# Kernel tuning notes

Hardware: AMD Instinct MI355X
Metric: run time of the kernel (lower is better)

Reference implementation:

```python
import jax, jax.numpy as jnp
import numpy as np
from itertools import permutations

B, Nm, S, K, H, OUT = 32, 128, 16, 4, 128, 1
LG, LI, LGL = 3, 2, 2  # num_layer, num_layer_id, num_layer_global
EPS = 1e-5


def _ln(x, g, b):
    m = jnp.mean(x, -1, keepdims=True)
    v = jnp.mean(jnp.square(x - m), -1, keepdims=True)
    return (x - m) * jax.lax.rsqrt(v + EPS) * g + b


def _block(x, W1, b1, W2, b2, g, bn):
    # Linear -> ReLU -> Linear -> LayerNorm -> ReLU
    h = jax.nn.relu(x @ W1 + b1)
    return jax.nn.relu(_ln(h @ W2 + b2, g, bn))


def setup_inputs() -> dict:
    key = jax.random.key(0)
    ks = iter(jax.random.split(key, 64))
    nrm = lambda shape, s=0.05: jax.random.normal(next(ks), shape, jnp.float32) * s
    x = nrm((B, Nm, 1), 1.0)
    adj = (jax.random.uniform(next(ks), (B, Nm, Nm)) < 0.05).astype(jnp.float32)
    # allperm: all permutations of [1..K-1] with 0 prepended, transposed -> (K, permdim)
    ap = np.array(list(permutations(range(1, K))), dtype=np.int32)
    ap = np.concatenate([np.zeros((ap.shape[0], 1), np.int32), ap], axis=1).T
    allperm = jnp.asarray(ap)
    Ssub = B * S
    base = jax.random.randint(next(ks), (Ssub,), 0, Nm - K)
    subgs = base[:, None] + jnp.arange(K, dtype=jnp.int32)[None, :]  # distinct nodes per subgraph
    num_subg = jnp.full((B,), S, jnp.int32)
    num_node = jnp.full((B,), Nm, jnp.int32)
    d = dict(x=x, adj=adj,
             idemb=nrm((K + 2, H)),
             in_W1=nrm((1, H)), in_b1=jnp.zeros((H,)), in_W2=nrm((H, H)), in_b2=jnp.zeros((H,)),
             in_g=jnp.ones((H,)), in_bn=jnp.zeros((H,)),
             gW1=nrm((LG, H, H)), gb1=jnp.zeros((LG, H)), gW2=nrm((LG, H, H)), gb2=jnp.zeros((LG, H)),
             gg=jnp.ones((LG, H)), gbn=jnp.zeros((LG, H)),
             iW1=nrm((LI, H, H)), ib1=jnp.zeros((LI, H)), iW2=nrm((LI, H, H)), ib2=jnp.zeros((LI, H)),
             ig=jnp.ones((LI, H)), ibn=jnp.zeros((LI, H)),
             glW1=nrm((LGL, H, H)), glb1=jnp.zeros((LGL, H)), glW2=nrm((LGL, H, H)), glb2=jnp.zeros((LGL, H)),
             glg=jnp.ones((LGL, H)), glbn=jnp.zeros((LGL, H)),
             s1_W=nrm((H, H)), s1_b=jnp.zeros((H,)), s2_W=nrm((H, H)), s2_b=jnp.zeros((H,)),
             rW1=nrm((H, H)), rb1=jnp.zeros((H,)), rW2=nrm((H, H)), rb2=jnp.zeros((H,)),
             rg=jnp.ones((H,)), rbn=jnp.zeros((H,)),
             out_W=nrm((H, OUT)), out_b=jnp.zeros((OUT,)),
             subgs=subgs, num_subg=num_subg, num_node=num_node, allperm=allperm)
    return d


def reference(x, adj, idemb, in_W1, in_b1, in_W2, in_b2, in_g, in_bn,
              gW1, gb1, gW2, gb2, gg, gbn,
              iW1, ib1, iW2, ib2, ig, ibn,
              glW1, glb1, glW2, glb2, glg, glbn,
              s1_W, s1_b, s2_W, s2_b,
              rW1, rb1, rW2, rb2, rg, rbn,
              out_W, out_b, subgs, num_subg, num_node, allperm):
    Bsz, N = x.shape[0], x.shape[1]
    Ssub, k = subgs.shape
    permdim = allperm.shape[1]
    # input embedding MLP
    h = _block(x, in_W1, in_b1, in_W2, in_b2, in_g, in_bn)  # (B, Nm, H)
    Hd = h.shape[-1]
    # subgraph -> graph batch map (ns_b = S per graph; Ssub static)
    subgbatch = jnp.repeat(jnp.arange(Bsz), num_subg, total_repeat_length=Ssub)
    # identity labeling: z starts as ones, labeled nodes get idemb(allperm[pos])
    lb = jnp.repeat(jnp.arange(Ssub), k)          # label batch (subgraph idx)
    lnodes = subgs.reshape(-1)                    # node ids within graph
    ni = jnp.tile(jnp.arange(k), Ssub)            # position within subgraph
    vals = idemb[allperm[ni]]                     # (Ssub*k, permdim, H)
    z = jnp.ones((Ssub, N, permdim, Hd), x.dtype)
    z = z.at[lb, lnodes].multiply(vals)
    # graph message passing on full graphs
    for l in range(gW1.shape[0]):
        m = jnp.einsum('bij,bjd->bid', adj, h)
        h = h + _block(m, gW1[l], gb1[l], gW2[l], gb2[l], gg[l], gbn[l])
    hs = h[subgbatch]        # (Ssub, Nm, H)
    sadj = adj[subgbatch]    # (Ssub, Nm, Nm)
    # id message passing over permutation channels
    for l in range(iW1.shape[0]):
        m = jnp.einsum('bij,bjpd->bipd', sadj, z)
        z = z + _block(m, iW1[l], ib1[l], iW2[l], ib2[l], ig[l], ibn[l])
    # zero out padded (null) nodes
    null_mask = jnp.arange(N)[None, :] >= num_node[:, None]  # (B, Nm)
    z = jnp.where(null_mask[subgbatch][:, :, None, None], 0.0, z)
    z = jax.nn.relu(z.mean(axis=2) @ s1_W + s1_b)  # setmlp1, (Ssub, Nm, H)
    hs = hs + z
    for l in range(glW1.shape[0]):
        m = jnp.einsum('bij,bjd->bid', sadj, hs)
        hs = hs + _block(m, glW1[l], glb1[l], glW2[l], glb2[l], glg[l], glbn[l])
    hs = jax.nn.relu(hs.sum(axis=1) @ s2_W + s2_b)  # setmlp2, (Ssub, H)
    pooled = jax.ops.segment_max(hs, subgbatch, num_segments=Bsz)  # global max pool
    pooled = pooled + _block(pooled, rW1, rb1, rW2, rb2, rg, rbn)  # setmlp3 (1 layer)
    return pooled @ out_W + out_b  # (B, OUT)
```

## Files before the change

### kernel.cpp

```cpp
#include <hip/hip_runtime.h>
#include <hip/hip_bf16.h>
#include <string.h>

typedef __hip_bfloat16 bf16;
typedef short v8s __attribute__((ext_vector_type(8)));
typedef float v4f __attribute__((ext_vector_type(4)));

#define H_ 128
#define P_ 6
#define K_ 4

__device__ __forceinline__ float s2f(short s) {
    unsigned int u = ((unsigned int)(unsigned short)s) << 16;
    float f; __builtin_memcpy(&f, &u, 4); return f;
}
__device__ __forceinline__ short f2s(float v) {
    bf16 h = __float2bfloat16(v);
    short s; __builtin_memcpy(&s, &h, 2); return s;
}
__device__ __forceinline__ v4f MFMA(v8s a, v8s b, v4f c) {
    return __builtin_amdgcn_mfma_f32_16x16x32_bf16(a, b, c, 0, 0, 0);
}

__global__ __launch_bounds__(128) void k_prep(const float* __restrict__ adj,
    float* __restrict__ degf, bf16* __restrict__ adjb,
    const float* __restrict__ iW1, const float* __restrict__ iW2,
    const float* __restrict__ glW1, const float* __restrict__ glW2,
    const float* __restrict__ in_W2, const float* __restrict__ gW1,
    const float* __restrict__ gW2, const float* __restrict__ s1_W,
    bf16* __restrict__ WT, bf16* __restrict__ WT2, bf16* __restrict__ s1Wt)
{
    __shared__ float red[128];
    const int b = blockIdx.x, t = threadIdx.x;
    if (b < 4096) {
        float a = adj[(size_t)b * 128 + t];
        adjb[(size_t)b * 128 + t] = __float2bfloat16(a);
        red[t] = a;
        __syncthreads();
        for (int s = 64; s > 0; s >>= 1) {
            if (t < s) red[t] += red[t + s];
            __syncthreads();
        }
        if (t == 0) degf[b] = red[0];
    } else if (b < 5120) {
        const int bb = b - 4096, w = bb >> 7, n = bb & 127;
        const float* arr[8] = {iW1, iW2, iW1 + 16384, iW2 + 16384,
                               glW1, glW2, glW1 + 16384, glW2 + 16384};
        WT[(size_t)w * 16384 + n * 128 + t] = __float2bfloat16(arr[w][t * 128 + n]);
    } else if (b < 6144) {
        const int bb = b - 5120, w = bb >> 7, n = bb & 127;
        const float* arr[8] = {in_W2, gW1, gW2, gW1 + 16384,
                               gW2 + 16384, gW1 + 32768, gW2 + 32768, in_W2};
        WT2[(size_t)w * 16384 + n * 128 + t] = __float2bfloat16(arr[w][t * 128 + n]);
    } else {
        const int n = b - 6144;
        s1Wt[n * 128 + t] = __float2bfloat16(s1_W[t * 128 + n]);
    }
}

__global__ __launch_bounds__(256) void k_id1h(
    const float* __restrict__ adj, const float* __restrict__ degf,
    const int* __restrict__ subgs, const int* __restrict__ allperm,
    const float* __restrict__ idemb, bf16* __restrict__ outb,
    const bf16* __restrict__ W1t, const float* __restrict__ b1,
    const bf16* __restrict__ W2t, const float* __restrict__ b2,
    const float* __restrict__ gam, const float* __restrict__ bet,
    const float* __restrict__ x, const bf16* __restrict__ adjb,
    const float* __restrict__ inW1, const float* __restrict__ inb1,
    const bf16* __restrict__ inW2t, const float* __restrict__ inb2,
    const float* __restrict__ ing, const float* __restrict__ inbn,
    const bf16* __restrict__ WTg,
    const float* __restrict__ gb1, const float* __restrict__ gb2,
    const float* __restrict__ gg, const float* __restrict__ gbn,
    float* __restrict__ hb)
{
    __shared__ __align__(16) short sB[128][136];
    __shared__ float sP[15][128];
    const int t = threadIdx.x;
    const int wave = t >> 6, lane = t & 63, quad = lane >> 4, l16 = lane & 15;
    const int wrow = wave << 5;

    if (blockIdx.x < 3072) {
        const int bi = blockIdx.x;
        const int b_s = bi / 6, p = bi - b_s * 6;
        const int g = b_s >> 4;
        float (*sE)[128] = sP;

        int nodeq[K_];
        #pragma unroll
        for (int q = 0; q < K_; ++q) nodeq[q] = subgs[b_s * K_ + q];

        for (int u = t; u < K_ * 128; u += 256) {
            const int q = u >> 7, f = u & 127;
            sE[q][f] = idemb[(size_t)allperm[q * P_ + p] * H_ + f] - 1.f;
        }
        __syncthreads();

        {
            const int i = t >> 1, half = (t & 1) * 64;
            const int gi = g * 128 + i;
            const float dg = degf[gi];
            float aq[K_];
            #pragma unroll
            for (int q = 0; q < K_; ++q) aq[q] = adj[(size_t)gi * 128 + nodeq[q]];
            #pragma unroll
            for (int f = 0; f < 64; ++f) {
                float v = dg;
                #pragma unroll
                for (int q = 0; q < K_; ++q) v = fmaf(aq[q], sE[q][half + f], v);
                sB[i][half + f] = f2s(v);
            }
        }
        __syncthreads();

        v4f acc[2][8];
        #pragma unroll
        for (int mt = 0; mt < 2; ++mt)
            #pragma unroll
            for (int nt = 0; nt < 8; ++nt) acc[mt][nt] = (v4f){0.f, 0.f, 0.f, 0.f};
        #pragma unroll
        for (int kk = 0; kk < 4; ++kk) {
            v8s a0 = *(const v8s*)&sB[wrow + l16][kk * 32 + quad * 8];
            v8s a1 = *(const v8s*)&sB[wrow + 16 + l16][kk * 32 + quad * 8];
            #pragma unroll
            for (int nt = 0; nt < 8; ++nt) {
                v8s b = *(const v8s*)(W1t + (nt * 16 + l16) * 128 + kk * 32 + quad * 8);
                acc[0][nt] = MFMA(a0, b, acc[0][nt]);
                acc[1][nt] = MFMA(a1, b, acc[1][nt]);
            }
        }
        #pragma unroll
        for (int nt = 0; nt < 8; ++nt) {
            float bb = b1[nt * 16 + l16];
            #pragma unroll
            for (int mt = 0; mt < 2; ++mt)
                #pragma unroll
                for (int r = 0; r < 4; ++r)
                    sB[wrow + mt * 16 + quad * 4 + r][nt * 16 + l16] = f2s(fmaxf(acc[mt][nt][r] + bb, 0.f));
        }
        #pragma unroll
        for (int mt = 0; mt < 2; ++mt)
            #pragma unroll
            for (int nt = 0; nt < 8; ++nt) acc[mt][nt] = (v4f){0.f, 0.f, 0.f, 0.f};
        #pragma unroll
        for (int kk = 0; kk < 4; ++kk) {
            v8s a0 = *(const v8s*)&sB[wrow + l16][kk * 32 + quad * 8];
            v8s a1 = *(const v8s*)&sB[wrow + 16 + l16][kk * 32 + quad * 8];
            #pragma unroll
            for (int nt = 0; nt < 8; ++nt) {
                v8s b = *(const v8s*)(W2t + (nt * 16 + l16) * 128 + kk * 32 + quad * 8);
                acc[0][nt] = MFMA(a0, b, acc[0][nt]);
                acc[1][nt] = MFMA(a1, b, acc[1][nt]);
            }
        }
        float bb2[8], gv[8], bv[8];
        #pragma unroll
        for (int nt = 0; nt < 8; ++nt) {
            int n = nt * 16 + l16;
            bb2[nt] = b2[n]; gv[nt] = gam[n]; bv[nt] = bet[n];
        }
        #pragma unroll
        for (int mt = 0; mt < 2; ++mt)
            #pragma unroll
            for (int r = 0; r < 4; ++r) {
                float s = 0.f, q = 0.f;
                #pragma unroll
                for (int nt = 0; nt < 8; ++nt) {
                    float u = acc[mt][nt][r] + bb2[nt];
                    acc[mt][nt][r] = u;
                    s += u; q += u * u;
                }
                #pragma unroll
                for (int d = 1; d < 16; d <<= 1) {
                    s += __shfl_xor(s, d);
                    q += __shfl_xor(q, d);
                }
                float mn = s * (1.f / 128.f);
                float rs = rsqrtf(q * (1.f / 128.f) - mn * mn + 1e-5f);
                #pragma unroll
                for (int nt = 0; nt < 8; ++nt) {
                    float v = fmaxf((acc[mt][nt][r] - mn) * rs * gv[nt] + bv[nt], 0.f);
                    sB[wrow + mt * 16 + quad * 4 + r][nt * 16 + l16] = f2s(v + 1.0f);
                }
            }
        __syncthreads();
        {
            const int f = t >> 1, nh = (t & 1) * 64;
            const short* flat = &sB[0][0];
            bf16* dst = outb + (size_t)bi * 16384 + (size_t)f * 128 + nh;
            #pragma unroll
            for (int u = 0; u < 8; ++u) {
                v8s pk;
                #pragma unroll
                for (int e = 0; e < 8; ++e) pk[e] = flat[(nh + u * 8 + e) * 136 + f];
                *(v8s*)(dst + u * 8) = pk;
            }
        }
        return;
    }

    const int g = blockIdx.x - 3072;

    for (int u = t; u < 15 * 128; u += 256) {
        const int a = u >> 7, n = u & 127;
        const float* src;
        if (a == 0) src = inb2;
        else if (a == 1) src = ing;
        else if (a == 2) src = inbn;
        else {
            const int l = (a - 3) >> 2, pp = (a - 3) & 3;
            src = (pp == 0) ? gb1 + l * 128 : (pp == 1) ? gb2 + l * 128
                : (pp == 2) ? gg + l * 128 : gbn + l * 128;
        }
        sP[a][n] = src[n];
    }

    v8s aA[2][4];
    {
        const bf16* ar = adjb + (size_t)g * 16384;
        #pragma unroll
        for (int mt = 0; mt < 2; ++mt)
            #pragma unroll
            for (int kk = 0; kk < 4; ++kk)
                aA[mt][kk] = *(const v8s*)(ar + (size_t)(wrow + mt * 16 + l16) * 128 + kk * 32 + quad * 8);
    }

    {
        const int i = t >> 1, half = (t & 1) * 64;
        const float xv = x[(size_t)g * 128 + i];
        #pragma unroll
        for (int fb = 0; fb < 64; fb += 8) {
            v8s pk;
            #pragma unroll
            for (int e = 0; e < 8; ++e)
                pk[e] = f2s(fmaxf(fmaf(xv, inW1[half + fb + e], inb1[half + fb + e]), 0.f));
            *(v8s*)&sB[i][half + fb] = pk;
        }
    }
    v4f acc[2][8];
    #pragma unroll
    for (int mt = 0; mt < 2; ++mt)
        #pragma unroll
        for (int nt = 0; nt < 8; ++nt) acc[mt][nt] = (v4f){0.f, 0.f, 0.f, 0.f};
    #pragma unroll
    for (int kk = 0; kk < 4; ++kk) {
        v8s a0 = *(const v8s*)&sB[wrow + l16][kk * 32 + quad * 8];
        v8s a1 = *(const v8s*)&sB[wrow + 16 + l16][kk * 32 + quad * 8];
        #pragma unroll
        for (int nt = 0; nt < 8; ++nt) {
            v8s b = *(const v8s*)(inW2t + (nt * 16 + l16) * 128 + kk * 32 + quad * 8);
            acc[0][nt] = MFMA(a0, b, acc[0][nt]);
            acc[1][nt] = MFMA(a1, b, acc[1][nt]);
        }
    }
    __syncthreads();
    float hs_reg[2][8][4];
    #pragma unroll
    for (int mt = 0; mt < 2; ++mt)
        #pragma unroll
        for (int r = 0; r < 4; ++r) {
            float s = 0.f, qq = 0.f;
            #pragma unroll
            for (int nt = 0; nt < 8; ++nt) {
                float u = acc[mt][nt][r] + sP[0][nt * 16 + l16];
                acc[mt][nt][r] = u;
                s += u; qq += u * u;
            }
            #pragma unroll
            for (int d = 1; d < 16; d <<= 1) {
                s += __shfl_xor(s, d);
                qq += __shfl_xor(qq, d);
            }
            float mn = s * (1.f / 128.f);
            float rs = rsqrtf(qq * (1.f / 128.f) - mn * mn + 1e-5f);
            const int i = wrow + mt * 16 + quad * 4 + r;
            #pragma unroll
            for (int nt = 0; nt < 8; ++nt) {
                const int n = nt * 16 + l16;
                float v = fmaxf((acc[mt][nt][r] - mn) * rs * sP[1][n] + sP[2][n], 0.f);
                hs_reg[mt][nt][r] = v;
                sB[n][i] = f2s(v);
            }
        }
    __syncthreads();

    for (int l = 0; l < 3; ++l) {
        const bf16* W1t_ = WTg + (size_t)(2 * l) * 16384;
        const bf16* W2t_ = WTg + (size_t)(2 * l + 1) * 16384;
        #pragma unroll
        for (int mt = 0; mt < 2; ++mt)
            #pragma unroll
            for (int nt = 0; nt < 8; ++nt) acc[mt][nt] = (v4f){0.f, 0.f, 0.f, 0.f};
        #pragma unroll
        for (int kk = 0; kk < 4; ++kk)
            #pragma unroll
            for (int nt = 0; nt < 8; ++nt) {
                v8s b = *(const v8s*)&sB[nt * 16 + l16][kk * 32 + quad * 8];
                acc[0][nt] = MFMA(aA[0][kk], b, acc[0][nt]);
                acc[1][nt] = MFMA(aA[1][kk], b, acc[1][nt]);
            }
        __syncthreads();
        #pragma unroll
        for (int nt = 0; nt < 8; ++nt)
            #pragma unroll
            for (int mt = 0; mt < 2; ++mt)
                #pragma unroll
                for (int r = 0; r < 4; ++r)
                    sB[wrow + mt * 16 + quad * 4 + r][nt * 16 + l16] = f2s(acc[mt][nt][r]);
        #pragma unroll
        for (int mt = 0; mt < 2; ++mt)
            #pragma unroll
            for (int nt = 0; nt < 8; ++nt) acc[mt][nt] = (v4f){0.f, 0.f, 0.f, 0.f};
        #pragma unroll
        for (int kk = 0; kk < 4; ++kk) {
            v8s a0 = *(const v8s*)&sB[wrow + l16][kk * 32 + quad * 8];
            v8s a1 = *(const v8s*)&sB[wrow + 16 + l16][kk * 32 + quad * 8];
            #pragma unroll
            for (int nt = 0; nt < 8; ++nt) {
                v8s b = *(const v8s*)(W1t_ + (nt * 16 + l16) * 128 + kk * 32 + quad * 8);
                acc[0][nt] = MFMA(a0, b, acc[0][nt]);
                acc[1][nt] = MFMA(a1, b, acc[1][nt]);
            }
        }
        #pragma unroll
        for (int nt = 0; nt < 8; ++nt) {
            float bb = sP[3 + 4 * l + 0][nt * 16 + l16];
            #pragma unroll
            for (int mt = 0; mt < 2; ++mt)
                #pragma unroll
                for (int r = 0; r < 4; ++r)
                    sB[wrow + mt * 16 + quad * 4 + r][nt * 16 + l16] = f2s(fmaxf(acc[mt][nt][r] + bb, 0.f));
        }
        #pragma unroll
        for (int mt = 0; mt < 2; ++mt)
            #pragma unroll
            for (int nt = 0; nt < 8; ++nt) acc[mt][nt] = (v4f){0.f, 0.f, 0.f, 0.f};
        #pragma unroll
        for (int kk = 0; kk < 4; ++kk) {
            v8s a0 = *(const v8s*)&sB[wrow + l16][kk * 32 + quad * 8];
            v8s a1 = *(const v8s*)&sB[wrow + 16 + l16][kk * 32 + quad * 8];
            #pragma unroll
            for (int nt = 0; nt < 8; ++nt) {
                v8s b = *(const v8s*)(W2t_ + (nt * 16 + l16) * 128 + kk * 32 + quad * 8);
                acc[0][nt] = MFMA(a0, b, acc[0][nt]);
                acc[1][nt] = MFMA(a1, b, acc[1][nt]);
            }
        }
        __syncthreads();
        #pragma unroll
        for (int mt = 0; mt < 2; ++mt)
            #pragma unroll
            for (int r = 0; r < 4; ++r) {
                float s = 0.f, qq = 0.f;
                #pragma unroll
                for (int nt = 0; nt < 8; ++nt) {
                    float u = acc[mt][nt][r] + sP[3 + 4 * l + 1][nt * 16 + l16];
                    acc[mt][nt][r] = u;
                    s += u; qq += u * u;
                }
                #pragma unroll
                for (int d = 1; d < 16; d <<= 1) {
                    s += __shfl_xor(s, d);
                    qq += __shfl_xor(qq, d);
                }
                float mn = s * (1.f / 128.f);
                float rs = rsqrtf(qq * (1.f / 128.f) - mn * mn + 1e-5f);
                const int i = wrow + mt * 16 + quad * 4 + r;
                #pragma unroll
                for (int nt = 0; nt < 8; ++nt) {
                    const int n = nt * 16 + l16;
                    float v = fmaxf((acc[mt][nt][r] - mn) * rs * sP[3 + 4 * l + 2][n] + sP[3 + 4 * l + 3][n], 0.f);
                    float h2 = hs_reg[mt][nt][r] + v;
                    hs_reg[mt][nt][r] = h2;
                    sB[n][i] = f2s(h2);
                }
            }
        __syncthreads();
    }

    #pragma unroll
    for (int mt = 0; mt < 2; ++mt)
        #pragma unroll
        for (int nt = 0; nt < 8; ++nt)
            #pragma unroll
            for (int r = 0; r < 4; ++r) {
                const int i = wrow + mt * 16 + quad * 4 + r;
                const int n = nt * 16 + l16;
                hb[((size_t)(g * 128 + i)) * 128 + n] = hs_reg[mt][nt][r];
            }
}

__global__ __launch_bounds__(256) void k_id2_v9(
    const bf16* __restrict__ z2t, bf16* __restrict__ zm,
    const bf16* __restrict__ adjb, const int* __restrict__ num_node,
    const int* __restrict__ subgs, const int* __restrict__ allperm,
    const float* __restrict__ idemb,
    const bf16* __restrict__ W1t, const float* __restrict__ b1,
    const bf16* __restrict__ W2t, const float* __restrict__ b2,
    const float* __restrict__ gam, const float* __restrict__ bet)
{
    __shared__ __align__(16) short sB[128][136];
    __shared__ float sP[4][128];
    const int t = threadIdx.x;
    const int b_s = blockIdx.x;
    const int g = b_s >> 4;
    const int wave = t >> 6, lane = t & 63, quad = lane >> 4, l16 = lane & 15;
    const int wrow = wave << 5;

    #pragma unroll
    for (int u = 0; u < 2; ++u) {
        const int v = t + u * 256;
        const int a = v >> 7, n = v & 127;
        const float* src = (a == 0) ? b1 : (a == 1) ? b2 : (a == 2) ? gam : bet;
        sP[a][n] = src[n];
    }

    v8s aA[2][4];
    {
        const bf16* ar = adjb + (size_t)g * 16384;
        #pragma unroll
        for (int mt = 0; mt < 2; ++mt)
            #pragma unroll
            for (int kk = 0; kk < 4; ++kk)
                aA[mt][kk] = *(const v8s*)(ar + (size_t)(wrow + mt * 16 + l16) * 128 + kk * 32 + quad * 8);
    }
    int nodeq[K_];
    #pragma unroll
    for (int q = 0; q < K_; ++q) nodeq[q] = subgs[b_s * K_ + q];

    float macc[2][8][4];
    #pragma unroll
    for (int mt = 0; mt < 2; ++mt)
        #pragma unroll
        for (int nt = 0; nt < 8; ++nt)
            #pragma unroll
            for (int r = 0; r < 4; ++r) macc[mt][nt][r] = 0.f;

    const int sf = t >> 1, shalf = (t & 1) * 64;

    for (int p = 0; p < P_; ++p) {
        {
            const bf16* src = z2t + ((size_t)(b_s * P_ + p)) * 16384 + (size_t)sf * 128 + shalf;
            #pragma unroll
            for (int u = 0; u < 8; ++u)
                *(v8s*)&sB[sf][shalf + u * 8] = *(const v8s*)(src + u * 8);
        }
        __syncthreads();
        if (t < 128) {
            #pragma unroll
            for (int q = 0; q < K_; ++q) {
                float e = idemb[(size_t)allperm[q * P_ + p] * H_ + t] - 1.f;
                short* cell = &sB[t][nodeq[q]];
                *cell = f2s(s2f(*cell) + e);
            }
        }
        __syncthreads();
        #pragma unroll
        for (int mt = 0; mt < 2; ++mt)
            #pragma unroll
            for (int nt = 0; nt < 8; ++nt) {
                const int n = nt * 16 + l16;
                #pragma unroll
                for (int r = 0; r < 4; ++r)
                    macc[mt][nt][r] += s2f(sB[n][wrow + mt * 16 + quad * 4 + r]);
            }
        v4f acc[2][8];
        #pragma unroll
        for (int mt = 0; mt < 2; ++mt)
            #pragma unroll
            for (int nt = 0; nt < 8; ++nt) acc[mt][nt] = (v4f){0.f, 0.f, 0.f, 0.f};
        #pragma unroll
        for (int kk = 0; kk < 4; ++kk)
            #pragma unroll
            for (int nt = 0; nt < 8; ++nt) {
                v8s b = *(const v8s*)&sB[nt * 16 + l16][kk * 32 + quad * 8];
                acc[0][nt] = MFMA(aA[0][kk], b, acc[0][nt]);
                acc[1][nt] = MFMA(aA[1][kk], b, acc[1][nt]);
            }
        __syncthreads();
        #pragma unroll
        for (int nt = 0; nt < 8; ++nt)
            #pragma unroll
            for (int mt = 0; mt < 2; ++mt)
                #pragma unroll
                for (int r = 0; r < 4; ++r)
                    sB[wrow + mt * 16 + quad * 4 + r][nt * 16 + l16] = f2s(acc[mt][nt][r]);
        #pragma unroll
        for (int mt = 0; mt < 2; ++mt)
            #pragma unroll
            for (int nt = 0; nt < 8; ++nt) acc[mt][nt] = (v4f){0.f, 0.f, 0.f, 0.f};
        #pragma unroll
        for (int kk = 0; kk < 4; ++kk) {
            v8s a0 = *(const v8s*)&sB[wrow + l16][kk * 32 + quad * 8];
            v8s a1 = *(const v8s*)&sB[wrow + 16 + l16][kk * 32 + quad * 8];
            #pragma unroll
            for (int nt = 0; nt < 8; ++nt) {
                v8s b = *(const v8s*)(W1t + (nt * 16 + l16) * 128 + kk * 32 + quad * 8);
                acc[0][nt] = MFMA(a0, b, acc[0][nt]);
                acc[1][nt] = MFMA(a1, b, acc[1][nt]);
            }
        }
        #pragma unroll
        for (int nt = 0; nt < 8; ++nt) {
            float bb = sP[0][nt * 16 + l16];
            #pragma unroll
            for (int mt = 0; mt < 2; ++mt)
                #pragma unroll
                for (int r = 0; r < 4; ++r)
                    sB[wrow + mt * 16 + quad * 4 + r][nt * 16 + l16] = f2s(fmaxf(acc[mt][nt][r] + bb, 0.f));
        }
        #pragma unroll
        for (int mt = 0; mt < 2; ++mt)
            #pragma unroll
            for (int nt = 0; nt < 8; ++nt) acc[mt][nt] = (v4f){0.f, 0.f, 0.f, 0.f};
        #pragma unroll
        for (int kk = 0; kk < 4; ++kk) {
            v8s a0 = *(const v8s*)&sB[wrow + l16][kk * 32 + quad * 8];
            v8s a1 = *(const v8s*)&sB[wrow + 16 + l16][kk * 32 + quad * 8];
            #pragma unroll
            for (int nt = 0; nt < 8; ++nt) {
                v8s b = *(const v8s*)(W2t + (nt * 16 + l16) * 128 + kk * 32 + quad * 8);
                acc[0][nt] = MFMA(a0, b, acc[0][nt]);
                acc[1][nt] = MFMA(a1, b, acc[1][nt]);
            }
        }
        #pragma unroll
        for (int mt = 0; mt < 2; ++mt)
            #pragma unroll
            for (int r = 0; r < 4; ++r) {
                float s = 0.f, qq = 0.f;
                #pragma unroll
                for (int nt = 0; nt < 8; ++nt) {
                    float u = acc[mt][nt][r] + sP[1][nt * 16 + l16];
                    acc[mt][nt][r] = u;
                    s += u; qq += u * u;
                }
                #pragma unroll
                for (int d = 1; d < 16; d <<= 1) {
                    s += __shfl_xor(s, d);
                    qq += __shfl_xor(qq, d);
                }
                float mn = s * (1.f / 128.f);
                float rs = rsqrtf(qq * (1.f / 128.f) - mn * mn + 1e-5f);
                #pragma unroll
                for (int nt = 0; nt < 8; ++nt) {
                    const int n = nt * 16 + l16;
                    macc[mt][nt][r] += fmaxf((acc[mt][nt][r] - mn) * rs * sP[2][n] + sP[3][n], 0.f);
                }
            }
        __syncthreads();
    }
    const int nn = num_node[g];
    #pragma unroll
    for (int mt = 0; mt < 2; ++mt)
        #pragma unroll
        for (int nt = 0; nt < 8; ++nt)
            #pragma unroll
            for (int r = 0; r < 4; ++r) {
                const int i = wrow + mt * 16 + quad * 4 + r;
                const int n = nt * 16 + l16;
                float v = (i >= nn) ? 0.f : macc[mt][nt][r] * (1.f / 6.f);
                zm[((size_t)(b_s * 128 + i)) * 128 + n] = __float2bfloat16(v);
            }
}

__global__ __launch_bounds__(256) void k_gl_fused(
    const bf16* __restrict__ zm, const float* __restrict__ hb,
    const bf16* __restrict__ adjb,
    const bf16* __restrict__ s1Wt, const float* __restrict__ s1_b,
    const bf16* __restrict__ WTgl,
    const float* __restrict__ glb1, const float* __restrict__ glb2,
    const float* __restrict__ glg, const float* __restrict__ glbn,
    float* __restrict__ hsum)
{
    __shared__ __align__(16) short sB[128][136];
    __shared__ float sP[9][128];
    const int t = threadIdx.x;
    const int b_s = blockIdx.x;
    const int g = b_s >> 4;
    const int wave = t >> 6, lane = t & 63, quad = lane >> 4, l16 = lane & 15;
    const int wrow = wave << 5;

    for (int u = t; u < 9 * 128; u += 256) {
        const int a = u >> 7, n = u & 127;
        const float* src =
            (a == 0) ? glb1 : (a == 1) ? glb2 : (a == 2) ? glg : (a == 3) ? glbn :
            (a == 4) ? glb1 + 128 : (a == 5) ? glb2 + 128 : (a == 6) ? glg + 128 :
            (a == 7) ? glbn + 128 : s1_b;
        sP[a][n] = src[n];
    }

    v8s aA[2][4];
    {
        const bf16* ar = adjb + (size_t)g * 16384;
        #pragma unroll
        for (int mt = 0; mt < 2; ++mt)
            #pragma unroll
            for (int kk = 0; kk < 4; ++kk)
                aA[mt][kk] = *(const v8s*)(ar + (size_t)(wrow + mt * 16 + l16) * 128 + kk * 32 + quad * 8);
    }

    v4f acc[2][8];
    #pragma unroll
    for (int mt = 0; mt < 2; ++mt)
        #pragma unroll
        for (int nt = 0; nt < 8; ++nt) acc[mt][nt] = (v4f){0.f, 0.f, 0.f, 0.f};
    #pragma unroll
    for (int kk = 0; kk < 4; ++kk) {
        v8s a0 = *(const v8s*)(zm + ((size_t)(b_s * 128) + wrow + l16) * 128 + kk * 32 + quad * 8);
        v8s a1 = *(const v8s*)(zm + ((size_t)(b_s * 128) + wrow + 16 + l16) * 128 + kk * 32 + quad * 8);
        #pragma unroll
        for (int nt = 0; nt < 8; ++nt) {
            v8s b = *(const v8s*)(s1Wt + (nt * 16 + l16) * 128 + kk * 32 + quad * 8);
            acc[0][nt] = MFMA(a0, b, acc[0][nt]);
            acc[1][nt] = MFMA(a1, b, acc[1][nt]);
        }
    }
    __syncthreads();
    float hs_reg[2][8][4];
    #pragma unroll
    for (int mt = 0; mt < 2; ++mt)
        #pragma unroll
        for (int nt = 0; nt < 8; ++nt)
            #pragma unroll
            for (int r = 0; r < 4; ++r) {
                const int i = wrow + mt * 16 + quad * 4 + r;
                const int n = nt * 16 + l16;
                float v = fmaxf(acc[mt][nt][r] + sP[8][n], 0.f);
                v += hb[((size_t)(g * 128 + i)) * 128 + n];
                hs_reg[mt][nt][r] = v;
                sB[n][i] = f2s(v);
            }
    __syncthreads();

    for (int l = 0; l < 2; ++l) {
        const bf16* W1t = WTgl + (size_t)(2 * l) * 16384;
        const bf16* W2t = WTgl + (size_t)(2 * l + 1) * 16384;
        #pragma unroll
        for (int mt = 0; mt < 2; ++mt)
            #pragma unroll
            for (int nt = 0; nt < 8; ++nt) acc[mt][nt] = (v4f){0.f, 0.f, 0.f, 0.f};
        #pragma unroll
        for (int kk = 0; kk < 4; ++kk)
            #pragma unroll
            for (int nt = 0; nt < 8; ++nt) {
                v8s b = *(const v8s*)&sB[nt * 16 + l16][kk * 32 + quad * 8];
                acc[0][nt] = MFMA(aA[0][kk], b, acc[0][nt]);
                acc[1][nt] = MFMA(aA[1][kk], b, acc[1][nt]);
            }
        __syncthreads();
        #pragma unroll
        for (int nt = 0; nt < 8; ++nt)
            #pragma unroll
            for (int mt = 0; mt < 2; ++mt)
                #pragma unroll
                for (int r = 0; r < 4; ++r)
                    sB[wrow + mt * 16 + quad * 4 + r][nt * 16 + l16] = f2s(acc[mt][nt][r]);
        #pragma unroll
        for (int mt = 0; mt < 2; ++mt)
            #pragma unroll
            for (int nt = 0; nt < 8; ++nt) acc[mt][nt] = (v4f){0.f, 0.f, 0.f, 0.f};
        #pragma unroll
        for (int kk = 0; kk < 4; ++kk) {
            v8s a0 = *(const v8s*)&sB[wrow + l16][kk * 32 + quad * 8];
            v8s a1 = *(const v8s*)&sB[wrow + 16 + l16][kk * 32 + quad * 8];
            #pragma unroll
            for (int nt = 0; nt < 8; ++nt) {
                v8s b = *(const v8s*)(W1t + (nt * 16 + l16) * 128 + kk * 32 + quad * 8);
                acc[0][nt] = MFMA(a0, b, acc[0][nt]);
                acc[1][nt] = MFMA(a1, b, acc[1][nt]);
            }
        }
        #pragma unroll
        for (int nt = 0; nt < 8; ++nt) {
            float bb = sP[4 * l + 0][nt * 16 + l16];
            #pragma unroll
            for (int mt = 0; mt < 2; ++mt)
                #pragma unroll
                for (int r = 0; r < 4; ++r)
                    sB[wrow + mt * 16 + quad * 4 + r][nt * 16 + l16] = f2s(fmaxf(acc[mt][nt][r] + bb, 0.f));
        }
        #pragma unroll
        for (int mt = 0; mt < 2; ++mt)
            #pragma unroll
            for (int nt = 0; nt < 8; ++nt) acc[mt][nt] = (v4f){0.f, 0.f, 0.f, 0.f};
        #pragma unroll
        for (int kk = 0; kk < 4; ++kk) {
            v8s a0 = *(const v8s*)&sB[wrow + l16][kk * 32 + quad * 8];
            v8s a1 = *(const v8s*)&sB[wrow + 16 + l16][kk * 32 + quad * 8];
            #pragma unroll
            for (int nt = 0; nt < 8; ++nt) {
                v8s b = *(const v8s*)(W2t + (nt * 16 + l16) * 128 + kk * 32 + quad * 8);
                acc[0][nt] = MFMA(a0, b, acc[0][nt]);
                acc[1][nt] = MFMA(a1, b, acc[1][nt]);
            }
        }
        __syncthreads();
        #pragma unroll
        for (int mt = 0; mt < 2; ++mt)
            #pragma unroll
            for (int r = 0; r < 4; ++r) {
                float s = 0.f, qq = 0.f;
                #pragma unroll
                for (int nt = 0; nt < 8; ++nt) {
                    float u = acc[mt][nt][r] + sP[4 * l + 1][nt * 16 + l16];
                    acc[mt][nt][r] = u;
                    s += u; qq += u * u;
                }
                #pragma unroll
                for (int d = 1; d < 16; d <<= 1) {
                    s += __shfl_xor(s, d);
                    qq += __shfl_xor(qq, d);
                }
                float mn = s * (1.f / 128.f);
                float rs = rsqrtf(qq * (1.f / 128.f) - mn * mn + 1e-5f);
                const int i = wrow + mt * 16 + quad * 4 + r;
                #pragma unroll
                for (int nt = 0; nt < 8; ++nt) {
                    const int n = nt * 16 + l16;
                    float v = fmaxf((acc[mt][nt][r] - mn) * rs * sP[4 * l + 2][n] + sP[4 * l + 3][n], 0.f);
                    float h2 = hs_reg[mt][nt][r] + v;
                    hs_reg[mt][nt][r] = h2;
                    sB[n][i] = f2s(h2);
                }
            }
        __syncthreads();
    }

    float* sRedf = (float*)&sB[0][0];
    #pragma unroll
    for (int nt = 0; nt < 8; ++nt) {
        float part = 0.f;
        #pragma unroll
        for (int mt = 0; mt < 2; ++mt)
            #pragma unroll
            for (int r = 0; r < 4; ++r) part += hs_reg[mt][nt][r];
        sRedf[(wave * 4 + quad) * 128 + nt * 16 + l16] = part;
    }
    __syncthreads();
    if (t < 128) {
        float s = 0.f;
        #pragma unroll
        for (int r = 0; r < 16; ++r) s += sRedf[r * 128 + t];
        hsum[(size_t)b_s * 128 + t] = s;
    }
}

__global__ __launch_bounds__(128) void k_tail(const float* __restrict__ hsum,
    const float* __restrict__ s2W, const float* __restrict__ s2b,
    const float* __restrict__ rW1, const float* __restrict__ rb1,
    const float* __restrict__ rW2, const float* __restrict__ rb2,
    const float* __restrict__ rg, const float* __restrict__ rbn,
    const float* __restrict__ outW, const float* __restrict__ outb,
    float* __restrict__ out)
{
    __shared__ float sA[16][136];
    __shared__ float sV[128];
    __shared__ float red[128];
    const int g = blockIdx.x, hd = threadIdx.x;
    #pragma unroll
    for (int r = 0; r < 16; ++r) sA[r][hd] = hsum[((size_t)(g * 16 + r)) * 128 + hd];
    __syncthreads();
    float acc[16];
    #pragma unroll
    for (int r = 0; r < 16; ++r) acc[r] = s2b[hd];
    for (int k = 0; k < 128; k += 4) {
        float w0 = s2W[(k+0)*128+hd], w1 = s2W[(k+1)*128+hd], w2 = s2W[(k+2)*128+hd], w3 = s2W[(k+3)*128+hd];
        #pragma unroll
        for (int r = 0; r < 16; ++r) {
            float4 a = *(const float4*)&sA[r][k];
            acc[r] = fmaf(a.x, w0, acc[r]); acc[r] = fmaf(a.y, w1, acc[r]);
            acc[r] = fmaf(a.z, w2, acc[r]); acc[r] = fmaf(a.w, w3, acc[r]);
        }
    }
    float pool = -INFINITY;
    #pragma unroll
    for (int r = 0; r < 16; ++r) pool = fmaxf(pool, fmaxf(acc[r], 0.f));
    sV[hd] = pool;
    __syncthreads();
    float t1 = rb1[hd];
    for (int k = 0; k < 128; ++k) t1 = fmaf(sV[k], rW1[k * 128 + hd], t1);
    t1 = fmaxf(t1, 0.f);
    red[hd] = t1;
    __syncthreads();
    float u = rb2[hd];
    for (int k = 0; k < 128; ++k) u = fmaf(red[k], rW2[k * 128 + hd], u);
    float* rs1 = (float*)&sA[0][0];
    float* rs2 = (float*)&sA[2][0];
    rs1[hd] = u; rs2[hd] = u * u;
    __syncthreads();
    for (int s = 64; s > 0; s >>= 1) {
        if (hd < s) { rs1[hd] += rs1[hd + s]; rs2[hd] += rs2[hd + s]; }
        __syncthreads();
    }
    float mn = rs1[0] * (1.f / 128.f);
    float var = rs2[0] * (1.f / 128.f) - mn * mn;
    float rstd = rsqrtf(var + 1e-5f);
    float p2 = fmaxf((u - mn) * rstd * rg[hd] + rbn[hd], 0.f) + sV[hd];
    __syncthreads();
    red[hd] = p2 * outW[hd];
    __syncthreads();
    for (int s = 64; s > 0; s >>= 1) {
        if (hd < s) red[hd] += red[hd + s];
        __syncthreads();
    }
    if (hd == 0) out[g] = red[0] + outb[0];
}

extern "C" void kernel_launch(void* const* d_in, const int* in_sizes, int n_in,
                              void* d_out, int out_size, void* d_ws, size_t ws_size,
                              hipStream_t stream)
{
    (void)in_sizes; (void)n_in; (void)out_size; (void)ws_size;
    const float* x     = (const float*)d_in[0];
    const float* adj   = (const float*)d_in[1];
    const float* idemb = (const float*)d_in[2];
    const float* in_W1 = (const float*)d_in[3];
    const float* in_b1 = (const float*)d_in[4];
    const float* in_W2 = (const float*)d_in[5];
    const float* in_b2 = (const float*)d_in[6];
    const float* in_g  = (const float*)d_in[7];
    const float* in_bn = (const float*)d_in[8];
    const float* gW1   = (const float*)d_in[9];
    const float* gb1   = (const float*)d_in[10];
    const float* gW2   = (const float*)d_in[11];
    const float* gb2   = (const float*)d_in[12];
    const float* gg    = (const float*)d_in[13];
    const float* gbn   = (const float*)d_in[14];
    const float* iW1   = (const float*)d_in[15];
    const float* ib1   = (const float*)d_in[16];
    const float* iW2   = (const float*)d_in[17];
    const float* ib2   = (const float*)d_in[18];
    const float* ig    = (const float*)d_in[19];
    const float* ibn   = (const float*)d_in[20];
    const float* glW1  = (const float*)d_in[21];
    const float* glb1  = (const float*)d_in[22];
    const float* glW2  = (const float*)d_in[23];
    const float* glb2  = (const float*)d_in[24];
    const float* glg   = (const float*)d_in[25];
    const float* glbn  = (const float*)d_in[26];
    const float* s1_W  = (const float*)d_in[27];
    const float* s1_b  = (const float*)d_in[28];
    const float* s2_W  = (const float*)d_in[29];
    const float* s2_b  = (const float*)d_in[30];
    const float* rW1   = (const float*)d_in[31];
    const float* rb1   = (const float*)d_in[32];
    const float* rW2   = (const float*)d_in[33];
    const float* rb2   = (const float*)d_in[34];
    const float* rg    = (const float*)d_in[35];
    const float* rbn   = (const float*)d_in[36];
    const float* out_W = (const float*)d_in[37];
    const float* out_b = (const float*)d_in[38];
    const int* subgs   = (const int*)d_in[39];
    const int* num_node= (const int*)d_in[41];
    const int* allperm = (const int*)d_in[42];

    const size_t MB_ = (size_t)512 * 128 * P_ * H_ * 2;
    char* w = (char*)d_ws;
    bf16*  mz     = (bf16*)(w);
    bf16*  s1Wt   = (bf16*)(w + 33554432ull);
    bf16*  zm     = (bf16*)(w + MB_);
    bf16*  WT     = (bf16*)(w + MB_ + 16777216ull);
    char*  wc     = w + MB_ + 16777216ull + 262144ull;
    float* hb     = (float*)(wc);
    bf16*  adjb   = (bf16*)(wc + 2097152ull);
    bf16*  WT2    = (bf16*)(wc + 3145728ull);
    float* hsum   = (float*)(wc + 4194304ull);
    bf16*  s1WtX  = (bf16*)(wc + 4456448ull);
    float* degf   = (float*)(wc + 4964352ull);
    float* outp   = (float*)d_out;
    (void)s1Wt;

    k_prep<<<6272, 128, 0, stream>>>(adj, degf, adjb,
        iW1, iW2, glW1, glW2, in_W2, gW1, gW2, s1_W,
        WT, WT2, s1WtX);

    k_id1h<<<3104, 256, 0, stream>>>(
        adj, degf, subgs, allperm, idemb, mz,
        WT, ib1, WT + 16384, ib2, ig, ibn,
        x, adjb, in_W1, in_b1,
        WT2, in_b2, in_g, in_bn,
        WT2 + 16384, gb1, gb2, gg, gbn, hb);

    k_id2_v9<<<512, 256, 0, stream>>>(mz, zm, adjb, num_node, subgs, allperm, idemb,
        WT + 2 * 16384, ib1 + 128, WT + 3 * 16384, ib2 + 128, ig + 128, ibn + 128);

    k_gl_fused<<<512, 256, 0, stream>>>(zm, hb, adjb, s1WtX, s1_b,
        WT + 4 * 16384, glb1, glb2, glg, glbn, hsum);

    k_tail<<<32, 128, 0, stream>>>(hsum, s2_W, s2_b, rW1, rb1, rW2, rb2,
        rg, rbn, out_W, out_b, outp);
}
```

Baseline: 611.2 us.

## Split combined id1/h kernel into two kernels with double-buffered LDS for h path

The merged kernel that handled both the id-layer-1 blocks and the 32 global h blocks becomes two launches: a 32-block h kernel and a 3072-block id1 kernel. The h kernel now uses two separate LDS buffers (transposed hs and message/activation), which removes some barriers. The id1 kernel drops the large sP array in favour of a small sE array, so it has a smaller LDS footprint and may fit more blocks per CU. The cost is an extra launch, and the 32 long h blocks now run serially before id1 instead of overlapping with it.

```diff
diff --git a/kernel.cpp b/kernel.cpp
--- a/kernel.cpp
+++ b/kernel.cpp
@@ -58,13 +58,7 @@
     }
 }
 
-__global__ __launch_bounds__(256) void k_id1h(
-    const float* __restrict__ adj, const float* __restrict__ degf,
-    const int* __restrict__ subgs, const int* __restrict__ allperm,
-    const float* __restrict__ idemb, bf16* __restrict__ outb,
-    const bf16* __restrict__ W1t, const float* __restrict__ b1,
-    const bf16* __restrict__ W2t, const float* __restrict__ b2,
-    const float* __restrict__ gam, const float* __restrict__ bet,
+__global__ __launch_bounds__(256) void k_h_fused(
     const float* __restrict__ x, const bf16* __restrict__ adjb,
     const float* __restrict__ inW1, const float* __restrict__ inb1,
     const bf16* __restrict__ inW2t, const float* __restrict__ inb2,
@@ -74,132 +68,13 @@
     const float* __restrict__ gg, const float* __restrict__ gbn,
     float* __restrict__ hb)
 {
-    __shared__ __align__(16) short sB[128][136];
+    __shared__ __align__(16) short sHsT[128][136];
+    __shared__ __align__(16) short sM[128][136];
     __shared__ float sP[15][128];
     const int t = threadIdx.x;
+    const int g = blockIdx.x;
     const int wave = t >> 6, lane = t & 63, quad = lane >> 4, l16 = lane & 15;
     const int wrow = wave << 5;
-
-    if (blockIdx.x < 3072) {
-        const int bi = blockIdx.x;
-        const int b_s = bi / 6, p = bi - b_s * 6;
-        const int g = b_s >> 4;
-        float (*sE)[128] = sP;
-
-        int nodeq[K_];
-        #pragma unroll
-        for (int q = 0; q < K_; ++q) nodeq[q] = subgs[b_s * K_ + q];
-
-        for (int u = t; u < K_ * 128; u += 256) {
-            const int q = u >> 7, f = u & 127;
-            sE[q][f] = idemb[(size_t)allperm[q * P_ + p] * H_ + f] - 1.f;
-        }
-        __syncthreads();
-
-        {
-            const int i = t >> 1, half = (t & 1) * 64;
-            const int gi = g * 128 + i;
-            const float dg = degf[gi];
-            float aq[K_];
-            #pragma unroll
-            for (int q = 0; q < K_; ++q) aq[q] = adj[(size_t)gi * 128 + nodeq[q]];
-            #pragma unroll
-            for (int f = 0; f < 64; ++f) {
-                float v = dg;
-                #pragma unroll
-                for (int q = 0; q < K_; ++q) v = fmaf(aq[q], sE[q][half + f], v);
-                sB[i][half + f] = f2s(v);
-            }
-        }
-        __syncthreads();
-
-        v4f acc[2][8];
-        #pragma unroll
-        for (int mt = 0; mt < 2; ++mt)
-            #pragma unroll
-            for (int nt = 0; nt < 8; ++nt) acc[mt][nt] = (v4f){0.f, 0.f, 0.f, 0.f};
-        #pragma unroll
-        for (int kk = 0; kk < 4; ++kk) {
-            v8s a0 = *(const v8s*)&sB[wrow + l16][kk * 32 + quad * 8];
-            v8s a1 = *(const v8s*)&sB[wrow + 16 + l16][kk * 32 + quad * 8];
-            #pragma unroll
-            for (int nt = 0; nt < 8; ++nt) {
-                v8s b = *(const v8s*)(W1t + (nt * 16 + l16) * 128 + kk * 32 + quad * 8);
-                acc[0][nt] = MFMA(a0, b, acc[0][nt]);
-                acc[1][nt] = MFMA(a1, b, acc[1][nt]);
-            }
-        }
-        #pragma unroll
-        for (int nt = 0; nt < 8; ++nt) {
-            float bb = b1[nt * 16 + l16];
-            #pragma unroll
-            for (int mt = 0; mt < 2; ++mt)
-                #pragma unroll
-                for (int r = 0; r < 4; ++r)
-                    sB[wrow + mt * 16 + quad * 4 + r][nt * 16 + l16] = f2s(fmaxf(acc[mt][nt][r] + bb, 0.f));
-        }
-        #pragma unroll
-        for (int mt = 0; mt < 2; ++mt)
-            #pragma unroll
-            for (int nt = 0; nt < 8; ++nt) acc[mt][nt] = (v4f){0.f, 0.f, 0.f, 0.f};
-        #pragma unroll
-        for (int kk = 0; kk < 4; ++kk) {
-            v8s a0 = *(const v8s*)&sB[wrow + l16][kk * 32 + quad * 8];
-            v8s a1 = *(const v8s*)&sB[wrow + 16 + l16][kk * 32 + quad * 8];
-            #pragma unroll
-            for (int nt = 0; nt < 8; ++nt) {
-                v8s b = *(const v8s*)(W2t + (nt * 16 + l16) * 128 + kk * 32 + quad * 8);
-                acc[0][nt] = MFMA(a0, b, acc[0][nt]);
-                acc[1][nt] = MFMA(a1, b, acc[1][nt]);
-            }
-        }
-        float bb2[8], gv[8], bv[8];
-        #pragma unroll
-        for (int nt = 0; nt < 8; ++nt) {
-            int n = nt * 16 + l16;
-            bb2[nt] = b2[n]; gv[nt] = gam[n]; bv[nt] = bet[n];
-        }
-        #pragma unroll
-        for (int mt = 0; mt < 2; ++mt)
-            #pragma unroll
-            for (int r = 0; r < 4; ++r) {
-                float s = 0.f, q = 0.f;
-                #pragma unroll
-                for (int nt = 0; nt < 8; ++nt) {
-                    float u = acc[mt][nt][r] + bb2[nt];
-                    acc[mt][nt][r] = u;
-                    s += u; q += u * u;
-                }
-                #pragma unroll
-                for (int d = 1; d < 16; d <<= 1) {
-                    s += __shfl_xor(s, d);
-                    q += __shfl_xor(q, d);
-                }
-                float mn = s * (1.f / 128.f);
-                float rs = rsqrtf(q * (1.f / 128.f) - mn * mn + 1e-5f);
-                #pragma unroll
-                for (int nt = 0; nt < 8; ++nt) {
-                    float v = fmaxf((acc[mt][nt][r] - mn) * rs * gv[nt] + bv[nt], 0.f);
-                    sB[wrow + mt * 16 + quad * 4 + r][nt * 16 + l16] = f2s(v + 1.0f);
-                }
-            }
-        __syncthreads();
-        {
-            const int f = t >> 1, nh = (t & 1) * 64;
-            const short* flat = &sB[0][0];
-            bf16* dst = outb + (size_t)bi * 16384 + (size_t)f * 128 + nh;
-            #pragma unroll
-            for (int u = 0; u < 8; ++u) {
-                v8s pk;
-                #pragma unroll
-                for (int e = 0; e < 8; ++e) pk[e] = flat[(nh + u * 8 + e) * 136 + f];
-                *(v8s*)(dst + u * 8) = pk;
-            }
-        }
-        return;
-    }
-
-    const int g = blockIdx.x - 3072;
 
     for (int u = t; u < 15 * 128; u += 256) {
         const int a = u >> 7, n = u & 127;
@@ -234,9 +109,11 @@
             #pragma unroll
             for (int e = 0; e < 8; ++e)
                 pk[e] = f2s(fmaxf(fmaf(xv, inW1[half + fb + e], inb1[half + fb + e]), 0.f));
-            *(v8s*)&sB[i][half + fb] = pk;
-        }
-    }
+            *(v8s*)&sM[i][half + fb] = pk;
+        }
+    }
+    __syncthreads();
+
     v4f acc[2][8];
     #pragma unroll
     for (int mt = 0; mt < 2; ++mt)
@@ -244,8 +121,8 @@
         for (int nt = 0; nt < 8; ++nt) acc[mt][nt] = (v4f){0.f, 0.f, 0.f, 0.f};
     #pragma unroll
     for (int kk = 0; kk < 4; ++kk) {
-        v8s a0 = *(const v8s*)&sB[wrow + l16][kk * 32 + quad * 8];
-        v8s a1 = *(const v8s*)&sB[wrow + 16 + l16][kk * 32 + quad * 8];
+        v8s a0 = *(const v8s*)&sM[wrow + l16][kk * 32 + quad * 8];
+        v8s a1 = *(const v8s*)&sM[wrow + 16 + l16][kk * 32 + quad * 8];
         #pragma unroll
         for (int nt = 0; nt < 8; ++nt) {
             v8s b = *(const v8s*)(inW2t + (nt * 16 + l16) * 128 + kk * 32 + quad * 8);
@@ -253,7 +130,6 @@
             acc[1][nt] = MFMA(a1, b, acc[1][nt]);
         }
     }
-    __syncthreads();
     float hs_reg[2][8][4];
     #pragma unroll
     for (int mt = 0; mt < 2; ++mt)
@@ -279,14 +155,14 @@
                 const int n = nt * 16 + l16;
                 float v = fmaxf((acc[mt][nt][r] - mn) * rs * sP[1][n] + sP[2][n], 0.f);
                 hs_reg[mt][nt][r] = v;
-                sB[n][i] = f2s(v);
+                sHsT[n][i] = f2s(v);
             }
         }
     __syncthreads();
 
     for (int l = 0; l < 3; ++l) {
-        const bf16* W1t_ = WTg + (size_t)(2 * l) * 16384;
-        const bf16* W2t_ = WTg + (size_t)(2 * l + 1) * 16384;
+        const bf16* W1t = WTg + (size_t)(2 * l) * 16384;
+        const bf16* W2t = WTg + (size_t)(2 * l + 1) * 16384;
         #pragma unroll
         for (int mt = 0; mt < 2; ++mt)
             #pragma unroll
@@ -295,29 +171,29 @@
         for (int kk = 0; kk < 4; ++kk)
             #pragma unroll
             for (int nt = 0; nt < 8; ++nt) {
-                v8s b = *(const v8s*)&sB[nt * 16 + l16][kk * 32 + quad * 8];
+                v8s b = *(const v8s*)&sHsT[nt * 16 + l16][kk * 32 + quad * 8];
                 acc[0][nt] = MFMA(aA[0][kk], b, acc[0][nt]);
                 acc[1][nt] = MFMA(aA[1][kk], b, acc[1][nt]);
             }
-        __syncthreads();
         #pragma unroll
         for (int nt = 0; nt < 8; ++nt)
             #pragma unroll
             for (int mt = 0; mt < 2; ++mt)
                 #pragma unroll
                 for (int r = 0; r < 4; ++r)
-                    sB[wrow + mt * 16 + quad * 4 + r][nt * 16 + l16] = f2s(acc[mt][nt][r]);
+                    sM[wrow + mt * 16 + quad * 4 + r][nt * 16 + l16] = f2s(acc[mt][nt][r]);
+        __syncthreads();
         #pragma unroll
         for (int mt = 0; mt < 2; ++mt)
             #pragma unroll
             for (int nt = 0; nt < 8; ++nt) acc[mt][nt] = (v4f){0.f, 0.f, 0.f, 0.f};
         #pragma unroll
         for (int kk = 0; kk < 4; ++kk) {
-            v8s a0 = *(const v8s*)&sB[wrow + l16][kk * 32 + quad * 8];
-            v8s a1 = *(const v8s*)&sB[wrow + 16 + l16][kk * 32 + quad * 8];
-            #pragma unroll
-            for (int nt = 0; nt < 8; ++nt) {
-                v8s b = *(const v8s*)(W1t_ + (nt * 16 + l16) * 128 + kk * 32 + quad * 8);
+            v8s a0 = *(const v8s*)&sM[wrow + l16][kk * 32 + quad * 8];
+            v8s a1 = *(const v8s*)&sM[wrow + 16 + l16][kk * 32 + quad * 8];
+            #pragma unroll
+            for (int nt = 0; nt < 8; ++nt) {
+                v8s b = *(const v8s*)(W1t + (nt * 16 + l16) * 128 + kk * 32 + quad * 8);
                 acc[0][nt] = MFMA(a0, b, acc[0][nt]);
                 acc[1][nt] = MFMA(a1, b, acc[1][nt]);
             }
@@ -329,7 +205,7 @@
             for (int mt = 0; mt < 2; ++mt)
                 #pragma unroll
                 for (int r = 0; r < 4; ++r)
-                    sB[wrow + mt * 16 + quad * 4 + r][nt * 16 + l16] = f2s(fmaxf(acc[mt][nt][r] + bb, 0.f));
+                    sM[wrow + mt * 16 + quad * 4 + r][nt * 16 + l16] = f2s(fmaxf(acc[mt][nt][r] + bb, 0.f));
         }
         #pragma unroll
         for (int mt = 0; mt < 2; ++mt)
@@ -337,16 +213,15 @@
             for (int nt = 0; nt < 8; ++nt) acc[mt][nt] = (v4f){0.f, 0.f, 0.f, 0.f};
         #pragma unroll
         for (int kk = 0; kk < 4; ++kk) {
-            v8s a0 = *(const v8s*)&sB[wrow + l16][kk * 32 + quad * 8];
-            v8s a1 = *(const v8s*)&sB[wrow + 16 + l16][kk * 32 + quad * 8];
-            #pragma unroll
-            for (int nt = 0; nt < 8; ++nt) {
-                v8s b = *(const v8s*)(W2t_ + (nt * 16 + l16) * 128 + kk * 32 + quad * 8);
+            v8s a0 = *(const v8s*)&sM[wrow + l16][kk * 32 + quad * 8];
+            v8s a1 = *(const v8s*)&sM[wrow + 16 + l16][kk * 32 + quad * 8];
+            #pragma unroll
+            for (int nt = 0; nt < 8; ++nt) {
+                v8s b = *(const v8s*)(W2t + (nt * 16 + l16) * 128 + kk * 32 + quad * 8);
                 acc[0][nt] = MFMA(a0, b, acc[0][nt]);
                 acc[1][nt] = MFMA(a1, b, acc[1][nt]);
             }
         }
-        __syncthreads();
         #pragma unroll
         for (int mt = 0; mt < 2; ++mt)
             #pragma unroll
@@ -372,7 +247,7 @@
                     float v = fmaxf((acc[mt][nt][r] - mn) * rs * sP[3 + 4 * l + 2][n] + sP[3 + 4 * l + 3][n], 0.f);
                     float h2 = hs_reg[mt][nt][r] + v;
                     hs_reg[mt][nt][r] = h2;
-                    sB[n][i] = f2s(h2);
+                    sHsT[n][i] = f2s(h2);
                 }
             }
         __syncthreads();
@@ -388,6 +263,136 @@
                 const int n = nt * 16 + l16;
                 hb[((size_t)(g * 128 + i)) * 128 + n] = hs_reg[mt][nt][r];
             }
+}
+
+__global__ __launch_bounds__(256) void k_id1_fused(
+    const float* __restrict__ adj, const float* __restrict__ degf,
+    const int* __restrict__ subgs, const int* __restrict__ allperm,
+    const float* __restrict__ idemb, bf16* __restrict__ outb,
+    const bf16* __restrict__ W1t, const float* __restrict__ b1,
+    const bf16* __restrict__ W2t, const float* __restrict__ b2,
+    const float* __restrict__ gam, const float* __restrict__ bet)
+{
+    __shared__ __align__(16) short sB[128][136];
+    __shared__ float sE[K_][128];
+    const int t = threadIdx.x;
+    const int bi = blockIdx.x;
+    const int b_s = bi / 6, p = bi - b_s * 6;
+    const int g = b_s >> 4;
+    const int wave = t >> 6, lane = t & 63;
+    const int quad = lane >> 4, l16 = lane & 15;
+    const int wrow = wave << 5;
+
+    int nodeq[K_];
+    #pragma unroll
+    for (int q = 0; q < K_; ++q) nodeq[q] = subgs[b_s * K_ + q];
+
+    for (int u = t; u < K_ * 128; u += 256) {
+        const int q = u >> 7, f = u & 127;
+        sE[q][f] = idemb[(size_t)allperm[q * P_ + p] * H_ + f] - 1.f;
+    }
+    __syncthreads();
+
+    {
+        const int i = t >> 1, half = (t & 1) * 64;
+        const int gi = g * 128 + i;
+        const float dg = degf[gi];
+        float aq[K_];
+        #pragma unroll
+        for (int q = 0; q < K_; ++q) aq[q] = adj[(size_t)gi * 128 + nodeq[q]];
+        #pragma unroll
+        for (int f = 0; f < 64; ++f) {
+            float v = dg;
+            #pragma unroll
+            for (int q = 0; q < K_; ++q) v = fmaf(aq[q], sE[q][half + f], v);
+            sB[i][half + f] = f2s(v);
+        }
+    }
+    __syncthreads();
+
+    v4f acc[2][8];
+    #pragma unroll
+    for (int mt = 0; mt < 2; ++mt)
+        #pragma unroll
+        for (int nt = 0; nt < 8; ++nt) acc[mt][nt] = (v4f){0.f, 0.f, 0.f, 0.f};
+    #pragma unroll
+    for (int kk = 0; kk < 4; ++kk) {
+        v8s a0 = *(const v8s*)&sB[wrow + l16][kk * 32 + quad * 8];
+        v8s a1 = *(const v8s*)&sB[wrow + 16 + l16][kk * 32 + quad * 8];
+        #pragma unroll
+        for (int nt = 0; nt < 8; ++nt) {
+            v8s b = *(const v8s*)(W1t + (nt * 16 + l16) * 128 + kk * 32 + quad * 8);
+            acc[0][nt] = MFMA(a0, b, acc[0][nt]);
+            acc[1][nt] = MFMA(a1, b, acc[1][nt]);
+        }
+    }
+    #pragma unroll
+    for (int nt = 0; nt < 8; ++nt) {
+        float bb = b1[nt * 16 + l16];
+        #pragma unroll
+        for (int mt = 0; mt < 2; ++mt)
+            #pragma unroll
+            for (int r = 0; r < 4; ++r)
+                sB[wrow + mt * 16 + quad * 4 + r][nt * 16 + l16] = f2s(fmaxf(acc[mt][nt][r] + bb, 0.f));
+    }
+    #pragma unroll
+    for (int mt = 0; mt < 2; ++mt)
+        #pragma unroll
+        for (int nt = 0; nt < 8; ++nt) acc[mt][nt] = (v4f){0.f, 0.f, 0.f, 0.f};
+    #pragma unroll
+    for (int kk = 0; kk < 4; ++kk) {
+        v8s a0 = *(const v8s*)&sB[wrow + l16][kk * 32 + quad * 8];
+        v8s a1 = *(const v8s*)&sB[wrow + 16 + l16][kk * 32 + quad * 8];
+        #pragma unroll
+        for (int nt = 0; nt < 8; ++nt) {
+            v8s b = *(const v8s*)(W2t + (nt * 16 + l16) * 128 + kk * 32 + quad * 8);
+            acc[0][nt] = MFMA(a0, b, acc[0][nt]);
+            acc[1][nt] = MFMA(a1, b, acc[1][nt]);
+        }
+    }
+    float bb2[8], gv[8], bv[8];
+    #pragma unroll
+    for (int nt = 0; nt < 8; ++nt) {
+        int n = nt * 16 + l16;
+        bb2[nt] = b2[n]; gv[nt] = gam[n]; bv[nt] = bet[n];
+    }
+    #pragma unroll
+    for (int mt = 0; mt < 2; ++mt)
+        #pragma unroll
+        for (int r = 0; r < 4; ++r) {
+            float s = 0.f, q = 0.f;
+            #pragma unroll
+            for (int nt = 0; nt < 8; ++nt) {
+                float u = acc[mt][nt][r] + bb2[nt];
+                acc[mt][nt][r] = u;
+                s += u; q += u * u;
+            }
+            #pragma unroll
+            for (int d = 1; d < 16; d <<= 1) {
+                s += __shfl_xor(s, d);
+                q += __shfl_xor(q, d);
+            }
+            float mn = s * (1.f / 128.f);
+            float rs = rsqrtf(q * (1.f / 128.f) - mn * mn + 1e-5f);
+            #pragma unroll
+            for (int nt = 0; nt < 8; ++nt) {
+                float v = fmaxf((acc[mt][nt][r] - mn) * rs * gv[nt] + bv[nt], 0.f);
+                sB[wrow + mt * 16 + quad * 4 + r][nt * 16 + l16] = f2s(v + 1.0f);
+            }
+        }
+    __syncthreads();
+    {
+        const int f = t >> 1, nh = (t & 1) * 64;
+        const short* flat = &sB[0][0];
+        bf16* dst = outb + (size_t)bi * 16384 + (size_t)f * 128 + nh;
+        #pragma unroll
+        for (int u = 0; u < 8; ++u) {
+            v8s pk;
+            #pragma unroll
+            for (int e = 0; e < 8; ++e) pk[e] = flat[(nh + u * 8 + e) * 136 + f];
+            *(v8s*)(dst + u * 8) = pk;
+        }
+    }
 }
 
 __global__ __launch_bounds__(256) void k_id2_v9(
@@ -858,7 +863,6 @@
     const size_t MB_ = (size_t)512 * 128 * P_ * H_ * 2;
     char* w = (char*)d_ws;
     bf16*  mz     = (bf16*)(w);
-    bf16*  s1Wt   = (bf16*)(w + 33554432ull);
     bf16*  zm     = (bf16*)(w + MB_);
     bf16*  WT     = (bf16*)(w + MB_ + 16777216ull);
     char*  wc     = w + MB_ + 16777216ull + 262144ull;
@@ -869,19 +873,18 @@
     bf16*  s1WtX  = (bf16*)(wc + 4456448ull);
     float* degf   = (float*)(wc + 4964352ull);
     float* outp   = (float*)d_out;
-    (void)s1Wt;
 
     k_prep<<<6272, 128, 0, stream>>>(adj, degf, adjb,
         iW1, iW2, glW1, glW2, in_W2, gW1, gW2, s1_W,
         WT, WT2, s1WtX);
 
-    k_id1h<<<3104, 256, 0, stream>>>(
-        adj, degf, subgs, allperm, idemb, mz,
-        WT, ib1, WT + 16384, ib2, ig, ibn,
-        x, adjb, in_W1, in_b1,
+    k_h_fused<<<32, 256, 0, stream>>>(x, adjb, in_W1, in_b1,
         WT2, in_b2, in_g, in_bn,
         WT2 + 16384, gb1, gb2, gg, gbn, hb);
 
+    k_id1_fused<<<3072, 256, 0, stream>>>(adj, degf, subgs, allperm, idemb, mz,
+        WT, ib1, WT + 16384, ib2, ig, ibn);
+
     k_id2_v9<<<512, 256, 0, stream>>>(mz, zm, adjb, num_node, subgs, allperm, idemb,
         WT + 2 * 16384, ib1 + 128, WT + 3 * 16384, ib2 + 128, ig + 128, ibn + 128);
 
```

New measurement: 550.1 us. 10.0% less time.
